# Kernel optimization log

Measured on AMD Instinct MI355X. Metric: run time of the kernel, lower is better.

Reference implementation:

```python
import jax, jax.numpy as jnp
import numpy as np

N = 100000
E = 1600000
K = 3
DIMS = [64, 64, 64, 32, 16]


def setup_inputs() -> dict:
    key = jax.random.key(0)
    ks = jax.random.split(key, 12)
    inp = {
        "x": jax.random.normal(ks[0], (N, DIMS[0]), jnp.float32),
        "edge_index": jax.random.randint(ks[1], (2, E), 0, N, dtype=jnp.int64),
        "edge_weight": jax.random.uniform(ks[2], (E,), jnp.float32),
    }
    for i in range(4):
        scale = 1.0 / np.sqrt(DIMS[i] * K).astype(np.float32)
        inp[f"W{i+1}"] = jax.random.normal(ks[3 + 2 * i], (K, DIMS[i], DIMS[i + 1]), jnp.float32) * scale
        inp[f"b{i+1}"] = jnp.zeros((DIMS[i + 1],), jnp.float32)
    return inp


def _cheb_norm(edge_index, edge_weight, n):
    # PyG ChebConv norm with normalization='sym', lambda_max=2:
    # L = I - D^{-1/2} A D^{-1/2}; L_hat = 2L/lambda_max - I = -D^{-1/2} A D^{-1/2} (zero diag)
    row, col = edge_index[0], edge_index[1]
    w = jnp.where(row == col, 0.0, edge_weight)  # remove self loops
    deg = jax.ops.segment_sum(w, row, num_segments=n)
    dinv = jnp.where(deg > 0, jax.lax.rsqrt(deg), 0.0)  # inf -> 0 masking
    return -dinv[row] * w * dinv[col]


def _cheb_conv(x, edge_index, norm, W, b):
    row, col = edge_index[0], edge_index[1]
    n = x.shape[0]

    def prop(t):  # sparse L_hat @ t via gather + segment scatter-add
        return jax.ops.segment_sum(norm[:, None] * t[row], col, num_segments=n)

    Tx0 = x
    out = Tx0 @ W[0]
    Tx1 = prop(Tx0)
    out = out + Tx1 @ W[1]
    for k in range(2, W.shape[0]):
        Tx2 = 2.0 * prop(Tx1) - Tx0  # Chebyshev recurrence
        out = out + Tx2 @ W[k]
        Tx0, Tx1 = Tx1, Tx2
    return out + b


def reference(x, edge_index, edge_weight, W1, b1, W2, b2, W3, b3, W4, b4):
    norm = _cheb_norm(edge_index, edge_weight, x.shape[0])
    h = x
    for W, b in ((W1, b1), (W2, b2), (W3, b3), (W4, b4)):
        h = jax.nn.sigmoid(_cheb_conv(h, edge_index, norm, W, b))
    return h
```

## Files before the change

### kernel.cpp

```cpp
#include <hip/hip_runtime.h>
#include <math.h>


typedef __attribute__((ext_vector_type(8))) short short8_t;
typedef __attribute__((ext_vector_type(4))) short short4_t;
typedef __attribute__((ext_vector_type(4))) float f32x4;

#define NPP 512
#define FSH 9
#define CHUNK 2048

__device__ __forceinline__ float bf2f(short s) {
    return __int_as_float(((int)(unsigned short)s) << 16);
}
__device__ __forceinline__ short f2bf(float f) {
    unsigned u = __float_as_uint(f);
    return (short)((u + 0x7FFFu + ((u >> 16) & 1u)) >> 16);
}


__global__ __launch_bounds__(256) void f2b_kernel(
        const float* __restrict__ in, short* __restrict__ out, long m) {
    long i = ((long)blockIdx.x * 256 + threadIdx.x) * 4;
    if (i >= m) return;
    float4 v = *reinterpret_cast<const float4*>(in + i);
    short4_t s;
    s[0] = f2bf(v.x); s[1] = f2bf(v.y); s[2] = f2bf(v.z); s[3] = f2bf(v.w);
    *reinterpret_cast<short4_t*>(out + i) = s;
}


__global__ __launch_bounds__(256) void prep_kernel(
        const float* __restrict__ W1, const float* __restrict__ W2,
        const float* __restrict__ W3, const float* __restrict__ W4,
        short8_t* __restrict__ wpk1, short8_t* __restrict__ wpk2,
        short8_t* __restrict__ wpkm, short8_t* __restrict__ wpk4) {
    int idx = blockIdx.x * 256 + threadIdx.x;
    if (idx >= 4032) return;
    short8_t out;
    if (idx < 3072) {
        const float* W = (idx < 1536) ? W1 : W2;
        int f = (idx < 1536) ? idx : idx - 1536;
        int lane = f & 63, ct = (f >> 6) & 3, s = f >> 8;
        int li = lane & 15, lg = lane >> 4;
        int p = s >> 1;
        int col = ct * 16 + li;
#pragma unroll
        for (int e = 0; e < 8; ++e) {
            int k = (s & 1) * 32 + lg * 8 + e;
            int base = k * 64 + col;
            float v = (p == 0) ? W[base] - W[8192 + base]
                    : (p == 1) ? W[4096 + base]
                               : 2.0f * W[8192 + base];
            out[e] = f2bf(v);
        }
        ((idx < 1536) ? wpk1 : wpk2)[f] = out;
    } else if (idx < 3840) {
        int f = idx - 3072;
        int lane = f & 63, q = f >> 6;
        int s = q / 6, ct = q % 6;
        int li = lane & 15, lg = lane >> 4;
        int g = ct >> 1;
        int cl = (ct & 1) * 16 + li;
#pragma unroll
        for (int e = 0; e < 8; ++e) {
            int k = s * 32 + lg * 8 + e;
            int base = k * 32 + cl;
            float v = (g == 0) ? W3[base] - W3[4096 + base]
                    : (g == 1) ? W3[2048 + base]
                               : W3[4096 + base];
            out[e] = f2bf(v);
        }
        wpkm[f] = out;
    } else {
        int f = idx - 3840;
        int lane = f & 63, s = f >> 6;
        int li = lane & 15, lg = lane >> 4;
#pragma unroll
        for (int e = 0; e < 8; ++e) {
            int k = lg * 8 + e;
            int base = k * 16 + li;
            float v = (s == 0) ? W4[base] - W4[1024 + base]
                    : (s == 1) ? W4[512 + base]
                               : 2.0f * W4[1024 + base];
            out[e] = f2bf(v);
        }
        wpk4[f] = out;
    }
}


__global__ __launch_bounds__(256) void count_kernel(
        const int* __restrict__ row, const int* __restrict__ col,
        int* __restrict__ cntC, int* __restrict__ cntR, int P, int E) {
    __shared__ int hc[2][256], hr[2][256];
    for (int i = threadIdx.x; i < P; i += 256) {
        hc[0][i] = 0; hc[1][i] = 0; hr[0][i] = 0; hr[1][i] = 0;
    }
    __syncthreads();
    int cp = threadIdx.x & 1;
    int base = blockIdx.x * CHUNK;
    int lim = min(E, base + CHUNK);
    for (int e = base + threadIdx.x; e < lim; e += 256) {
        atomicAdd(&hc[cp][col[e] >> FSH], 1);
        atomicAdd(&hr[cp][row[e] >> FSH], 1);
    }
    __syncthreads();
    long o = (long)blockIdx.x * P;
    for (int i = threadIdx.x; i < P; i += 256) {
        cntC[o + i] = hc[0][i] + hc[1][i];
        cntR[o + i] = hr[0][i] + hr[1][i];
    }
}

__global__ __launch_bounds__(256) void colscan_kernel(
        int* __restrict__ cntC, int* __restrict__ cntR,
        int* __restrict__ ptotC, int* __restrict__ ptotR, int P, int B) {
    int bid = blockIdx.x;
    int* m; int* ptot; int p;
    if (bid < P) { m = cntC; ptot = ptotC; p = bid; }
    else         { m = cntR; ptot = ptotR; p = bid - P; }
    __shared__ int sh[256];
    int run = 0;
    for (int b0 = 0; b0 < B; b0 += 256) {
        int b = b0 + threadIdx.x;
        int v = (b < B) ? m[(long)b * P + p] : 0;
        sh[threadIdx.x] = v;
        __syncthreads();
        for (int o = 1; o < 256; o <<= 1) {
            int t = (threadIdx.x >= o) ? sh[threadIdx.x - o] : 0;
            __syncthreads();
            sh[threadIdx.x] += t;
            __syncthreads();
        }
        if (b < B) m[(long)b * P + p] = run + sh[threadIdx.x] - v;
        run += sh[255];
        __syncthreads();
    }
    if (threadIdx.x == 0) ptot[p] = run;
}

__global__ __launch_bounds__(256) void pscan_kernel(
        const int* __restrict__ ptotC, const int* __restrict__ ptotR,
        int* __restrict__ pofsC, int* __restrict__ pofsR,
        int* __restrict__ ofs, int P, int n, int E) {
    __shared__ int sh[256];
    int tid = threadIdx.x;
    int v = (tid < P) ? ptotC[tid] : 0;
    sh[tid] = v;
    __syncthreads();
    for (int o = 1; o < 256; o <<= 1) {
        int t = (tid >= o) ? sh[tid - o] : 0;
        __syncthreads();
        sh[tid] += t;
        __syncthreads();
    }
    if (tid < P) pofsC[tid] = sh[tid] - v;
    if (tid == 0) pofsC[P] = E;
    __syncthreads();
    v = (tid < P) ? ptotR[tid] : 0;
    sh[tid] = v;
    __syncthreads();
    for (int o = 1; o < 256; o <<= 1) {
        int t = (tid >= o) ? sh[tid - o] : 0;
        __syncthreads();
        sh[tid] += t;
        __syncthreads();
    }
    if (tid < P) pofsR[tid] = sh[tid] - v;
    if (tid == 0) { pofsR[P] = E; ofs[n] = E; }
}

__global__ __launch_bounds__(256) void scatter_kernel(
        const int* __restrict__ row, const int* __restrict__ col,
        const float* __restrict__ ew,
        const int* __restrict__ cntC, const int* __restrict__ cntR,
        const int* __restrict__ pofsC, const int* __restrict__ pofsR,
        int2* __restrict__ bufC, unsigned* __restrict__ bufR, int P, int E) {
    __shared__ int hc[256], hr[256];
    long o = (long)blockIdx.x * P;
    for (int i = threadIdx.x; i < P; i += 256) {
        hc[i] = pofsC[i] + cntC[o + i];
        hr[i] = pofsR[i] + cntR[o + i];
    }
    __syncthreads();
    int base = blockIdx.x * CHUNK;
    int lim = min(E, base + CHUNK);
    for (int e = base + threadIdx.x; e < lim; e += 256) {
        int r = row[e], c = col[e];
        float w = (r == c) ? 0.0f : ew[e];
        unsigned wb = __float_as_uint(w);
        int pc = atomicAdd(&hc[c >> FSH], 1);
        bufC[pc] = make_int2((int)(((unsigned)(c & (NPP - 1)) << 23) | (unsigned)r), (int)wb);
        int pr = atomicAdd(&hr[r >> FSH], 1);
        bufR[pr] = ((unsigned)(r & (NPP - 1)) << 23) | (wb >> 9);
    }
}

__global__ __launch_bounds__(512) void dinv_kernel(
        const unsigned* __restrict__ bufR, const int* __restrict__ rofs,
        float* __restrict__ dinv, int n) {
    int p = blockIdx.x;
    __shared__ float s[NPP];
    s[threadIdx.x] = 0.0f;
    __syncthreads();
    int beg = rofs[p], end = rofs[p + 1];
    for (int k = beg + threadIdx.x; k < end; k += 512) {
        unsigned u = bufR[k];
        atomicAdd(&s[u >> 23], __uint_as_float((u & 0x7FFFFFu) << 9));
    }
    __syncthreads();
    int node = (p << FSH) + threadIdx.x;
    if (node < n) {
        float d = s[threadIdx.x];
        dinv[node] = d > 0.0f ? rsqrtf(d) : 0.0f;
    }
}

__global__ __launch_bounds__(512) void fine_csr_kernel(
        const int2* __restrict__ bufC, const int* __restrict__ pofs,
        const float* __restrict__ dinv, int* __restrict__ ofs,
        int2* __restrict__ epk, int n) {
    int p = blockIdx.x;
    int tid = threadIdx.x;
    __shared__ int hist[NPP];
    __shared__ int sc[NPP];
    __shared__ float dc[NPP];
    hist[tid] = 0;
    int node = (p << FSH) + tid;
    dc[tid] = (node < n) ? dinv[node] : 0.0f;
    __syncthreads();
    int beg = pofs[p], end = pofs[p + 1];
    for (int k = beg + tid; k < end; k += 512)
        atomicAdd(&hist[((unsigned)bufC[k].x) >> 23], 1);
    __syncthreads();
    int v = hist[tid];
    sc[tid] = v;
    __syncthreads();
    for (int o = 1; o < 512; o <<= 1) {
        int t = (tid >= o) ? sc[tid - o] : 0;
        __syncthreads();
        sc[tid] += t;
        __syncthreads();
    }
    int mybase = beg + sc[tid] - v;
    if (node < n) ofs[node] = mybase;
    hist[tid] = mybase;
    __syncthreads();
    for (int k = beg + tid; k < end; k += 512) {
        int2 ed = bufC[k];
        unsigned key = (unsigned)ed.x;
        int fc = key >> 23;
        int r = (int)(key & 0x7FFFFFu);
        float w = __int_as_float(ed.y);
        float nrm = -dinv[r] * w * dc[fc];
        int pos = atomicAdd(&hist[fc], 1);
        epk[pos] = make_int2(r, __float_as_int(nrm));
    }
}


template <int D>
__global__ __launch_bounds__(256) void agg_kernel(
        const int* __restrict__ ofs, const int2* __restrict__ epk,
        const short* __restrict__ tb, short* __restrict__ outb, int n) {
    constexpr int LPN = D / 8;
    int idx = blockIdx.x * 256 + threadIdx.x;
    int node = idx / LPN;
    int l = idx % LPN;
    if (node >= n) return;
    int beg = ofs[node], end = ofs[node + 1];
    float a[8] = {0.f, 0.f, 0.f, 0.f, 0.f, 0.f, 0.f, 0.f};
    const short* tc = tb + l * 8;
    int k = beg;
    for (; k + 8 <= end; k += 8) {
        int2 ev[8];
        short8_t xv[8];
#pragma unroll
        for (int u = 0; u < 8; ++u) ev[u] = epk[k + u];
#pragma unroll
        for (int u = 0; u < 8; ++u)
            xv[u] = *reinterpret_cast<const short8_t*>(tc + (long)ev[u].x * D);
#pragma unroll
        for (int u = 0; u < 8; ++u) {
            float v = __int_as_float(ev[u].y);
#pragma unroll
            for (int j = 0; j < 8; ++j) a[j] = fmaf(v, bf2f(xv[u][j]), a[j]);
        }
    }
    for (; k + 4 <= end; k += 4) {
        int2 ev[4];
        short8_t xv[4];
#pragma unroll
        for (int u = 0; u < 4; ++u) ev[u] = epk[k + u];
#pragma unroll
        for (int u = 0; u < 4; ++u)
            xv[u] = *reinterpret_cast<const short8_t*>(tc + (long)ev[u].x * D);
#pragma unroll
        for (int u = 0; u < 4; ++u) {
            float v = __int_as_float(ev[u].y);
#pragma unroll
            for (int j = 0; j < 8; ++j) a[j] = fmaf(v, bf2f(xv[u][j]), a[j]);
        }
    }
    for (; k < end; ++k) {
        int2 e0 = epk[k];
        short8_t x0 = *reinterpret_cast<const short8_t*>(tc + (long)e0.x * D);
        float v = __int_as_float(e0.y);
#pragma unroll
        for (int j = 0; j < 8; ++j) a[j] = fmaf(v, bf2f(x0[j]), a[j]);
    }
    short8_t s;
#pragma unroll
    for (int j = 0; j < 8; ++j) s[j] = f2bf(a[j]);
    *reinterpret_cast<short8_t*>(outb + (long)node * D + l * 8) = s;
}


__global__ __launch_bounds__(256) void agg_dual_kernel(
        const int* __restrict__ ofs, const int2* __restrict__ epk,
        const short* __restrict__ tb, short* __restrict__ Q1b,
        short* __restrict__ Q2b, int n) {
    int idx = blockIdx.x * 256 + threadIdx.x;
    int node = idx >> 3;
    int l = idx & 7;
    if (node >= n) return;
    int beg = ofs[node], end = ofs[node + 1];
    float a[8] = {0.f, 0.f, 0.f, 0.f, 0.f, 0.f, 0.f, 0.f};
    const short* tc = tb + l * 8;
    int k = beg;
    for (; k + 8 <= end; k += 8) {
        int2 ev[8];
        short8_t xv[8];
#pragma unroll
        for (int u = 0; u < 8; ++u) ev[u] = epk[k + u];
#pragma unroll
        for (int u = 0; u < 8; ++u)
            xv[u] = *reinterpret_cast<const short8_t*>(tc + (long)ev[u].x * 64);
#pragma unroll
        for (int u = 0; u < 8; ++u) {
            float v = __int_as_float(ev[u].y);
#pragma unroll
            for (int j = 0; j < 8; ++j) a[j] = fmaf(v, bf2f(xv[u][j]), a[j]);
        }
    }
    for (; k + 4 <= end; k += 4) {
        int2 ev[4];
        short8_t xv[4];
#pragma unroll
        for (int u = 0; u < 4; ++u) ev[u] = epk[k + u];
#pragma unroll
        for (int u = 0; u < 4; ++u)
            xv[u] = *reinterpret_cast<const short8_t*>(tc + (long)ev[u].x * 64);
#pragma unroll
        for (int u = 0; u < 4; ++u) {
            float v = __int_as_float(ev[u].y);
#pragma unroll
            for (int j = 0; j < 8; ++j) a[j] = fmaf(v, bf2f(xv[u][j]), a[j]);
        }
    }
    for (; k < end; ++k) {
        int2 e0 = epk[k];
        short8_t x0 = *reinterpret_cast<const short8_t*>(tc + (long)e0.x * 64);
        float v = __int_as_float(e0.y);
#pragma unroll
        for (int j = 0; j < 8; ++j) a[j] = fmaf(v, bf2f(x0[j]), a[j]);
    }
    short* ob = (l < 4) ? Q1b : Q2b;
    long o = (long)node * 32 + (l & 3) * 8;
    short8_t s;
#pragma unroll
    for (int j = 0; j < 8; ++j) s[j] = f2bf(a[j]);
    *reinterpret_cast<short8_t*>(ob + o) = s;
}


__global__ __launch_bounds__(256) void agg_fin_kernel(
        const int* __restrict__ ofs, const int2* __restrict__ epk,
        const short* __restrict__ Q2b, const float* __restrict__ S,
        const short* __restrict__ Q1b, short* __restrict__ outb, int n) {
    int idx = blockIdx.x * 256 + threadIdx.x;
    int node = idx >> 2;
    int l = idx & 3;
    if (node >= n) return;
    int beg = ofs[node], end = ofs[node + 1];
    float a[8] = {0.f, 0.f, 0.f, 0.f, 0.f, 0.f, 0.f, 0.f};
    const short* tc = Q2b + l * 8;
    int k = beg;
    for (; k + 4 <= end; k += 4) {
        int2 ev[4];
        short8_t xv[4];
#pragma unroll
        for (int u = 0; u < 4; ++u) ev[u] = epk[k + u];
#pragma unroll
        for (int u = 0; u < 4; ++u)
            xv[u] = *reinterpret_cast<const short8_t*>(tc + (long)ev[u].x * 32);
#pragma unroll
        for (int u = 0; u < 4; ++u) {
            float v = __int_as_float(ev[u].y);
#pragma unroll
            for (int j = 0; j < 8; ++j) a[j] = fmaf(v, bf2f(xv[u][j]), a[j]);
        }
    }
    for (; k < end; ++k) {
        int2 e0 = epk[k];
        short8_t x0 = *reinterpret_cast<const short8_t*>(tc + (long)e0.x * 32);
        float v = __int_as_float(e0.y);
#pragma unroll
        for (int j = 0; j < 8; ++j) a[j] = fmaf(v, bf2f(x0[j]), a[j]);
    }
    long o = (long)node * 32 + l * 8;
    float4 s0 = *reinterpret_cast<const float4*>(S + o);
    float4 s1 = *reinterpret_cast<const float4*>(S + o + 4);
    short8_t q1 = *reinterpret_cast<const short8_t*>(Q1b + o);
    float sv[8] = {s0.x, s0.y, s0.z, s0.w, s1.x, s1.y, s1.z, s1.w};
    short8_t r;
#pragma unroll
    for (int j = 0; j < 8; ++j) {
        float z = sv[j] + bf2f(q1[j]) + 2.0f * a[j];
        r[j] = f2bf(1.0f / (1.0f + expf(-z)));
    }
    *reinterpret_cast<short8_t*>(outb + o) = r;
}


__global__ __launch_bounds__(256) void gemm3_mfma(
        const short* __restrict__ t0b, const short* __restrict__ t1b,
        const short* __restrict__ t2b, const short8_t* __restrict__ wpk,
        const float* __restrict__ b, short* __restrict__ outb, int n) {
    const int tid = threadIdx.x;
    const int wave = tid >> 6;
    const int lane = tid & 63;
    const int li = lane & 15;
    const int lg = lane >> 4;

    short8_t bfr[6][4];
#pragma unroll
    for (int s = 0; s < 6; ++s)
#pragma unroll
        for (int ct = 0; ct < 4; ++ct)
            bfr[s][ct] = wpk[(s * 4 + ct) * 64 + lane];

    float bias_v[4];
#pragma unroll
    for (int ct = 0; ct < 4; ++ct) bias_v[ct] = b[ct * 16 + li];

#pragma unroll
    for (int t = 0; t < 2; ++t) {
        int r0 = blockIdx.x * 128 + wave * 32 + t * 16;
        if (r0 >= n) continue;
        int rA = r0 + li;
        if (rA >= n) rA = n - 1;
        f32x4 acc[4] = {{0.f, 0.f, 0.f, 0.f}, {0.f, 0.f, 0.f, 0.f},
                        {0.f, 0.f, 0.f, 0.f}, {0.f, 0.f, 0.f, 0.f}};
#pragma unroll
        for (int s = 0; s < 6; ++s) {
            const short* src = (s < 2) ? t0b : (s < 4) ? t1b : t2b;
            int k = (s & 1) * 32 + lg * 8;
            short8_t a = *reinterpret_cast<const short8_t*>(src + (long)rA * 64 + k);
#pragma unroll
            for (int ct = 0; ct < 4; ++ct)
                acc[ct] = __builtin_amdgcn_mfma_f32_16x16x32_bf16(a, bfr[s][ct], acc[ct], 0, 0, 0);
        }
#pragma unroll
        for (int ct = 0; ct < 4; ++ct) {
#pragma unroll
            for (int reg = 0; reg < 4; ++reg) {
                int row = r0 + lg * 4 + reg;
                if (row < n) {
                    float z = acc[ct][reg] + bias_v[ct];
                    float res = 1.0f / (1.0f + expf(-z));
                    outb[(long)row * 64 + ct * 16 + li] = f2bf(res);
                }
            }
        }
    }
}

__global__ __launch_bounds__(256) void gemm_multi_mfma(
        const short* __restrict__ hb, const short8_t* __restrict__ wpk,
        const float* __restrict__ b, short* __restrict__ P12b,
        float* __restrict__ S, int n) {
    const int tid = threadIdx.x;
    const int wave = tid >> 6;
    const int lane = tid & 63;
    const int li = lane & 15;
    const int lg = lane >> 4;

    short8_t bfr[2][6];
#pragma unroll
    for (int s = 0; s < 2; ++s)
#pragma unroll
        for (int ct = 0; ct < 6; ++ct)
            bfr[s][ct] = wpk[(s * 6 + ct) * 64 + lane];

    float bS0 = b[li], bS1 = b[16 + li];

#pragma unroll
    for (int t = 0; t < 2; ++t) {
        int r0 = blockIdx.x * 128 + wave * 32 + t * 16;
        if (r0 >= n) continue;
        int rA = r0 + li;
        if (rA >= n) rA = n - 1;
        f32x4 acc[6] = {{0.f, 0.f, 0.f, 0.f}, {0.f, 0.f, 0.f, 0.f},
                        {0.f, 0.f, 0.f, 0.f}, {0.f, 0.f, 0.f, 0.f},
                        {0.f, 0.f, 0.f, 0.f}, {0.f, 0.f, 0.f, 0.f}};
#pragma unroll
        for (int s = 0; s < 2; ++s) {
            int k = s * 32 + lg * 8;
            short8_t a = *reinterpret_cast<const short8_t*>(hb + (long)rA * 64 + k);
#pragma unroll
            for (int ct = 0; ct < 6; ++ct)
                acc[ct] = __builtin_amdgcn_mfma_f32_16x16x32_bf16(a, bfr[s][ct], acc[ct], 0, 0, 0);
        }
#pragma unroll
        for (int ct = 0; ct < 6; ++ct) {
            int g = ct >> 1;
            int cl = (ct & 1) * 16 + li;
#pragma unroll
            for (int reg = 0; reg < 4; ++reg) {
                int row = r0 + lg * 4 + reg;
                if (row >= n) continue;
                float v = acc[ct][reg];
                if (g == 0) {
                    S[(long)row * 32 + cl] = v + ((ct & 1) ? bS1 : bS0);
                } else if (g == 1) {
                    P12b[(long)row * 64 + cl] = f2bf(v);
                } else {
                    P12b[(long)row * 64 + 32 + cl] = f2bf(v);
                }
            }
        }
    }
}

__global__ __launch_bounds__(256) void gemm4_mfma(
        const short* __restrict__ t0b, const short* __restrict__ t1b,
        const short* __restrict__ t2b, const short8_t* __restrict__ wpk,
        const float* __restrict__ b, float* __restrict__ out, int n) {
    const int tid = threadIdx.x;
    const int wave = tid >> 6;
    const int lane = tid & 63;
    const int li = lane & 15;
    const int lg = lane >> 4;

    short8_t bfr[3];
#pragma unroll
    for (int s = 0; s < 3; ++s) bfr[s] = wpk[s * 64 + lane];

    float bias_v = b[li];

#pragma unroll
    for (int t = 0; t < 2; ++t) {
        int r0 = blockIdx.x * 128 + wave * 32 + t * 16;
        if (r0 >= n) continue;
        int rA = r0 + li;
        if (rA >= n) rA = n - 1;
        f32x4 acc = {0.f, 0.f, 0.f, 0.f};
        int k = lg * 8;
        short8_t a0 = *reinterpret_cast<const short8_t*>(t0b + (long)rA * 32 + k);
        acc = __builtin_amdgcn_mfma_f32_16x16x32_bf16(a0, bfr[0], acc, 0, 0, 0);
        short8_t a1 = *reinterpret_cast<const short8_t*>(t1b + (long)rA * 32 + k);
        acc = __builtin_amdgcn_mfma_f32_16x16x32_bf16(a1, bfr[1], acc, 0, 0, 0);
        short8_t a2 = *reinterpret_cast<const short8_t*>(t2b + (long)rA * 32 + k);
        acc = __builtin_amdgcn_mfma_f32_16x16x32_bf16(a2, bfr[2], acc, 0, 0, 0);
#pragma unroll
        for (int reg = 0; reg < 4; ++reg) {
            int row = r0 + lg * 4 + reg;
            if (row < n) {
                float z = acc[reg] + bias_v;
                out[(long)row * 16 + li] = 1.0f / (1.0f + expf(-z));
            }
        }
    }
}


static inline int ceil_div_l(long a, long b) { return (int)((a + b - 1) / b); }

extern "C" void kernel_launch(void* const* d_in, const int* in_sizes, int n_in,
                              void* d_out, int out_size, void* d_ws, size_t ws_size,
                              hipStream_t stream) {
    const float* x  = (const float*)d_in[0];
    const int*   ei = (const int*)d_in[1];
    const float* ew = (const float*)d_in[2];
    const float* W1 = (const float*)d_in[3];  const float* b1 = (const float*)d_in[4];
    const float* W2 = (const float*)d_in[5];  const float* b2 = (const float*)d_in[6];
    const float* W3 = (const float*)d_in[7];  const float* b3 = (const float*)d_in[8];
    const float* W4 = (const float*)d_in[9];  const float* b4 = (const float*)d_in[10];

    const int E = in_sizes[2];
    const int n = in_sizes[0] / 64;
    const int* row = ei;
    const int* col = ei + E;
    const int P = (n + NPP - 1) / NPP;
    const int B = (E + CHUNK - 1) / CHUNK;

    char* ws = (char*)d_ws;
    size_t off = 0;
    auto alloc = [&](size_t bytes) -> void* {
        void* p = ws + off;
        off += (bytes + 255) & ~(size_t)255;
        return p;
    };
    int*      cntC = (int*)alloc((size_t)B * P * sizeof(int));
    int*      cntR = (int*)alloc((size_t)B * P * sizeof(int));
    int*      ptotC = (int*)alloc(256 * sizeof(int));
    int*      ptotR = (int*)alloc(256 * sizeof(int));
    int*      pofsC = (int*)alloc((256 + 1) * sizeof(int));
    int*      pofsR = (int*)alloc((256 + 1) * sizeof(int));
    float*    dinv = (float*)alloc((size_t)n * sizeof(float));
    int*      ofs  = (int*)alloc((size_t)(n + 1) * sizeof(int));
    int2*     bufC = (int2*)alloc((size_t)E * sizeof(int2));
    unsigned* bufR = (unsigned*)alloc((size_t)E * sizeof(unsigned));
    int2*     epk  = (int2*)alloc((size_t)E * sizeof(int2));
    short*    hbA  = (short*)alloc((size_t)n * 64 * sizeof(short));
    short*    hbB  = (short*)alloc((size_t)n * 64 * sizeof(short));
    short*    t1b  = (short*)alloc((size_t)n * 64 * sizeof(short));
    short*    Ub   = (short*)alloc((size_t)n * 64 * sizeof(short));
    float*    S    = (float*)alloc((size_t)n * 32 * sizeof(float));
    short8_t* wpk1 = (short8_t*)alloc(1536 * sizeof(short8_t));
    short8_t* wpk2 = (short8_t*)alloc(1536 * sizeof(short8_t));
    short8_t* wpkm = (short8_t*)alloc(768 * sizeof(short8_t));
    short8_t* wpk4 = (short8_t*)alloc(192 * sizeof(short8_t));
    if (off > ws_size) return;

    f2b_kernel<<<ceil_div_l((long)n * 16, 256), 256, 0, stream>>>(x, hbA, (long)n * 64);
    prep_kernel<<<16, 256, 0, stream>>>(W1, W2, W3, W4, wpk1, wpk2, wpkm, wpk4);

    count_kernel<<<B, 256, 0, stream>>>(row, col, cntC, cntR, P, E);
    colscan_kernel<<<2 * P, 256, 0, stream>>>(cntC, cntR, ptotC, ptotR, P, B);
    pscan_kernel<<<1, 256, 0, stream>>>(ptotC, ptotR, pofsC, pofsR, ofs, P, n, E);
    scatter_kernel<<<B, 256, 0, stream>>>(row, col, ew, cntC, cntR, pofsC, pofsR,
                                          bufC, bufR, P, E);
    dinv_kernel<<<P, 512, 0, stream>>>(bufR, pofsR, dinv, n);
    fine_csr_kernel<<<P, 512, 0, stream>>>(bufC, pofsC, dinv, ofs, epk, n);

    const int ab64 = ceil_div_l((long)n * 8, 256);
    const int ab32 = ceil_div_l((long)n * 4, 256);
    const int gb = ceil_div_l(n, 128);

    agg_kernel<64><<<ab64, 256, 0, stream>>>(ofs, epk, hbA, t1b, n);
    agg_kernel<64><<<ab64, 256, 0, stream>>>(ofs, epk, t1b, Ub, n);
    gemm3_mfma<<<gb, 256, 0, stream>>>(hbA, t1b, Ub, wpk1, b1, hbB, n);

    agg_kernel<64><<<ab64, 256, 0, stream>>>(ofs, epk, hbB, t1b, n);
    agg_kernel<64><<<ab64, 256, 0, stream>>>(ofs, epk, t1b, Ub, n);
    gemm3_mfma<<<gb, 256, 0, stream>>>(hbB, t1b, Ub, wpk2, b2, hbA, n);

    {
        short* P12b = t1b;
        short* Q1b  = Ub;
        short* Q2b  = Ub + (size_t)n * 32;
        short* hb3  = hbB;
        gemm_multi_mfma<<<gb, 256, 0, stream>>>(hbA, wpkm, b3, P12b, S, n);
        agg_dual_kernel<<<ab64, 256, 0, stream>>>(ofs, epk, P12b, Q1b, Q2b, n);
        agg_fin_kernel<<<ab32, 256, 0, stream>>>(ofs, epk, Q2b, S, Q1b, hb3, n);
    }

    agg_kernel<32><<<ab32, 256, 0, stream>>>(ofs, epk, hbB, t1b, n);
    agg_kernel<32><<<ab32, 256, 0, stream>>>(ofs, epk, t1b, Ub, n);
    gemm4_mfma<<<gb, 256, 0, stream>>>(hbB, t1b, Ub, wpk4, b4, (float*)d_out, n);
}
```

Baseline: 396.6 us.

## Pack CSR edges into 32-bit words and remap edge chunks by XCD

```diff
diff --git a/kernel.cpp b/kernel.cpp
--- a/kernel.cpp
+++ b/kernel.cpp
@@ -9,6 +9,7 @@
 #define NPP 512
 #define FSH 9
 #define CHUNK 2048
+#define NXCD 8
 
 __device__ __forceinline__ float bf2f(short s) {
     return __int_as_float(((int)(unsigned short)s) << 16);
@@ -16,6 +17,18 @@
 __device__ __forceinline__ short f2bf(float f) {
     unsigned u = __float_as_uint(f);
     return (short)((u + 0x7FFFu + ((u >> 16) & 1u)) >> 16);
+}
+
+__device__ __forceinline__ int chunk_of_block(int bid, int B) {
+    int xcd = bid & (NXCD - 1);
+    int i = bid >> 3;
+    int q = B >> 3, r = B & (NXCD - 1);
+    return (xcd < r) ? xcd * (q + 1) + i : r * (q + 1) + (xcd - r) * q + i;
+}
+
+__device__ __forceinline__ int epk_row(unsigned u) { return (int)(u & 0x1FFFFu); }
+__device__ __forceinline__ float epk_val(unsigned u) {
+    return __uint_as_float((u >> 17) << 17);
 }
 
 
@@ -98,15 +111,16 @@
         hc[0][i] = 0; hc[1][i] = 0; hr[0][i] = 0; hr[1][i] = 0;
     }
     __syncthreads();
+    int chunk = chunk_of_block(blockIdx.x, gridDim.x);
     int cp = threadIdx.x & 1;
-    int base = blockIdx.x * CHUNK;
+    int base = chunk * CHUNK;
     int lim = min(E, base + CHUNK);
     for (int e = base + threadIdx.x; e < lim; e += 256) {
         atomicAdd(&hc[cp][col[e] >> FSH], 1);
         atomicAdd(&hr[cp][row[e] >> FSH], 1);
     }
     __syncthreads();
-    long o = (long)blockIdx.x * P;
+    long o = (long)chunk * P;
     for (int i = threadIdx.x; i < P; i += 256) {
         cntC[o + i] = hc[0][i] + hc[1][i];
         cntR[o + i] = hr[0][i] + hr[1][i];
@@ -178,13 +192,14 @@
         const int* __restrict__ pofsC, const int* __restrict__ pofsR,
         int2* __restrict__ bufC, unsigned* __restrict__ bufR, int P, int E) {
     __shared__ int hc[256], hr[256];
-    long o = (long)blockIdx.x * P;
+    int chunk = chunk_of_block(blockIdx.x, gridDim.x);
+    long o = (long)chunk * P;
     for (int i = threadIdx.x; i < P; i += 256) {
         hc[i] = pofsC[i] + cntC[o + i];
         hr[i] = pofsR[i] + cntR[o + i];
     }
     __syncthreads();
-    int base = blockIdx.x * CHUNK;
+    int base = chunk * CHUNK;
     int lim = min(E, base + CHUNK);
     for (int e = base + threadIdx.x; e < lim; e += 256) {
         int r = row[e], c = col[e];
@@ -220,7 +235,7 @@
 __global__ __launch_bounds__(512) void fine_csr_kernel(
         const int2* __restrict__ bufC, const int* __restrict__ pofs,
         const float* __restrict__ dinv, int* __restrict__ ofs,
-        int2* __restrict__ epk, int n) {
+        unsigned* __restrict__ epk, int n) {
     int p = blockIdx.x;
     int tid = threadIdx.x;
     __shared__ int hist[NPP];
@@ -254,15 +269,17 @@
         int r = (int)(key & 0x7FFFFFu);
         float w = __int_as_float(ed.y);
         float nrm = -dinv[r] * w * dc[fc];
+        unsigned nb = __float_as_uint(nrm);
+        unsigned n15 = (nb + 0xFFFFu + ((nb >> 17) & 1u)) >> 17;
         int pos = atomicAdd(&hist[fc], 1);
-        epk[pos] = make_int2(r, __float_as_int(nrm));
+        epk[pos] = (n15 << 17) | (unsigned)r;
     }
 }
 
 
 template <int D>
 __global__ __launch_bounds__(256) void agg_kernel(
-        const int* __restrict__ ofs, const int2* __restrict__ epk,
+        const int* __restrict__ ofs, const unsigned* __restrict__ epk,
         const short* __restrict__ tb, short* __restrict__ outb, int n) {
     constexpr int LPN = D / 8;
     int idx = blockIdx.x * 256 + threadIdx.x;
@@ -274,39 +291,39 @@
     const short* tc = tb + l * 8;
     int k = beg;
     for (; k + 8 <= end; k += 8) {
-        int2 ev[8];
+        unsigned ev[8];
         short8_t xv[8];
 #pragma unroll
         for (int u = 0; u < 8; ++u) ev[u] = epk[k + u];
 #pragma unroll
         for (int u = 0; u < 8; ++u)
-            xv[u] = *reinterpret_cast<const short8_t*>(tc + (long)ev[u].x * D);
+            xv[u] = *reinterpret_cast<const short8_t*>(tc + (long)epk_row(ev[u]) * D);
 #pragma unroll
         for (int u = 0; u < 8; ++u) {
-            float v = __int_as_float(ev[u].y);
+            float v = epk_val(ev[u]);
 #pragma unroll
             for (int j = 0; j < 8; ++j) a[j] = fmaf(v, bf2f(xv[u][j]), a[j]);
         }
     }
     for (; k + 4 <= end; k += 4) {
-        int2 ev[4];
+        unsigned ev[4];
         short8_t xv[4];
 #pragma unroll
         for (int u = 0; u < 4; ++u) ev[u] = epk[k + u];
 #pragma unroll
         for (int u = 0; u < 4; ++u)
-            xv[u] = *reinterpret_cast<const short8_t*>(tc + (long)ev[u].x * D);
+            xv[u] = *reinterpret_cast<const short8_t*>(tc + (long)epk_row(ev[u]) * D);
 #pragma unroll
         for (int u = 0; u < 4; ++u) {
-            float v = __int_as_float(ev[u].y);
+            float v = epk_val(ev[u]);
 #pragma unroll
             for (int j = 0; j < 8; ++j) a[j] = fmaf(v, bf2f(xv[u][j]), a[j]);
         }
     }
     for (; k < end; ++k) {
-        int2 e0 = epk[k];
-        short8_t x0 = *reinterpret_cast<const short8_t*>(tc + (long)e0.x * D);
-        float v = __int_as_float(e0.y);
+        unsigned e0 = epk[k];
+        short8_t x0 = *reinterpret_cast<const short8_t*>(tc + (long)epk_row(e0) * D);
+        float v = epk_val(e0);
 #pragma unroll
         for (int j = 0; j < 8; ++j) a[j] = fmaf(v, bf2f(x0[j]), a[j]);
     }
@@ -318,7 +335,7 @@
 
 
 __global__ __launch_bounds__(256) void agg_dual_kernel(
-        const int* __restrict__ ofs, const int2* __restrict__ epk,
+        const int* __restrict__ ofs, const unsigned* __restrict__ epk,
         const short* __restrict__ tb, short* __restrict__ Q1b,
         short* __restrict__ Q2b, int n) {
     int idx = blockIdx.x * 256 + threadIdx.x;
@@ -330,39 +347,39 @@
     const short* tc = tb + l * 8;
     int k = beg;
     for (; k + 8 <= end; k += 8) {
-        int2 ev[8];
+        unsigned ev[8];
         short8_t xv[8];
 #pragma unroll
         for (int u = 0; u < 8; ++u) ev[u] = epk[k + u];
 #pragma unroll
         for (int u = 0; u < 8; ++u)
-            xv[u] = *reinterpret_cast<const short8_t*>(tc + (long)ev[u].x * 64);
+            xv[u] = *reinterpret_cast<const short8_t*>(tc + (long)epk_row(ev[u]) * 64);
 #pragma unroll
         for (int u = 0; u < 8; ++u) {
-            float v = __int_as_float(ev[u].y);
+            float v = epk_val(ev[u]);
 #pragma unroll
             for (int j = 0; j < 8; ++j) a[j] = fmaf(v, bf2f(xv[u][j]), a[j]);
         }
     }
     for (; k + 4 <= end; k += 4) {
-        int2 ev[4];
+        unsigned ev[4];
         short8_t xv[4];
 #pragma unroll
         for (int u = 0; u < 4; ++u) ev[u] = epk[k + u];
 #pragma unroll
         for (int u = 0; u < 4; ++u)
-            xv[u] = *reinterpret_cast<const short8_t*>(tc + (long)ev[u].x * 64);
+            xv[u] = *reinterpret_cast<const short8_t*>(tc + (long)epk_row(ev[u]) * 64);
 #pragma unroll
         for (int u = 0; u < 4; ++u) {
-            float v = __int_as_float(ev[u].y);
+            float v = epk_val(ev[u]);
 #pragma unroll
             for (int j = 0; j < 8; ++j) a[j] = fmaf(v, bf2f(xv[u][j]), a[j]);
         }
     }
     for (; k < end; ++k) {
-        int2 e0 = epk[k];
-        short8_t x0 = *reinterpret_cast<const short8_t*>(tc + (long)e0.x * 64);
-        float v = __int_as_float(e0.y);
+        unsigned e0 = epk[k];
+        short8_t x0 = *reinterpret_cast<const short8_t*>(tc + (long)epk_row(e0) * 64);
+        float v = epk_val(e0);
 #pragma unroll
         for (int j = 0; j < 8; ++j) a[j] = fmaf(v, bf2f(x0[j]), a[j]);
     }
@@ -376,7 +393,7 @@
 
 
 __global__ __launch_bounds__(256) void agg_fin_kernel(
-        const int* __restrict__ ofs, const int2* __restrict__ epk,
+        const int* __restrict__ ofs, const unsigned* __restrict__ epk,
         const short* __restrict__ Q2b, const float* __restrict__ S,
         const short* __restrict__ Q1b, short* __restrict__ outb, int n) {
     int idx = blockIdx.x * 256 + threadIdx.x;
@@ -388,24 +405,24 @@
     const short* tc = Q2b + l * 8;
     int k = beg;
     for (; k + 4 <= end; k += 4) {
-        int2 ev[4];
+        unsigned ev[4];
         short8_t xv[4];
 #pragma unroll
         for (int u = 0; u < 4; ++u) ev[u] = epk[k + u];
 #pragma unroll
         for (int u = 0; u < 4; ++u)
-            xv[u] = *reinterpret_cast<const short8_t*>(tc + (long)ev[u].x * 32);
+            xv[u] = *reinterpret_cast<const short8_t*>(tc + (long)epk_row(ev[u]) * 32);
 #pragma unroll
         for (int u = 0; u < 4; ++u) {
-            float v = __int_as_float(ev[u].y);
+            float v = epk_val(ev[u]);
 #pragma unroll
             for (int j = 0; j < 8; ++j) a[j] = fmaf(v, bf2f(xv[u][j]), a[j]);
         }
     }
     for (; k < end; ++k) {
-        int2 e0 = epk[k];
-        short8_t x0 = *reinterpret_cast<const short8_t*>(tc + (long)e0.x * 32);
-        float v = __int_as_float(e0.y);
+        unsigned e0 = epk[k];
+        short8_t x0 = *reinterpret_cast<const short8_t*>(tc + (long)epk_row(e0) * 32);
+        float v = epk_val(e0);
 #pragma unroll
         for (int j = 0; j < 8; ++j) a[j] = fmaf(v, bf2f(x0[j]), a[j]);
     }
@@ -613,7 +630,7 @@
     int*      ofs  = (int*)alloc((size_t)(n + 1) * sizeof(int));
     int2*     bufC = (int2*)alloc((size_t)E * sizeof(int2));
     unsigned* bufR = (unsigned*)alloc((size_t)E * sizeof(unsigned));
-    int2*     epk  = (int2*)alloc((size_t)E * sizeof(int2));
+    unsigned* epk  = (unsigned*)alloc((size_t)E * sizeof(unsigned));
     short*    hbA  = (short*)alloc((size_t)n * 64 * sizeof(short));
     short*    hbB  = (short*)alloc((size_t)n * 64 * sizeof(short));
     short*    t1b  = (short*)alloc((size_t)n * 64 * sizeof(short));
```

New measurement: 360.1 us. 1.1x faster.
